# Optimization experiments

Hardware: AMD Instinct MI355X
Metric: run time of the kernel (lower is better)

The kernel has to match this reference:

```python
import jax, jax.numpy as jnp
import numpy as np

TOP_K = 8


def setup_inputs() -> dict:
    key = jax.random.key(0)
    k1, k2 = jax.random.split(key)
    hidden_states = jax.random.normal(k1, (16384, 2048), dtype=jnp.float32)
    weight = jax.random.normal(k2, (64, 2048), dtype=jnp.float32) * 0.02
    return {"hidden_states": hidden_states, "weight": weight}


def reference(hidden_states, weight):
    # router_logits = F.linear(hidden_states, weight): [T, E]
    router_logits = jnp.einsum('th,eh->te', hidden_states, weight)
    # softmax in float32 as in the original
    router_probs = jax.nn.softmax(router_logits.astype(jnp.float32), axis=-1)
    router_top_values, router_indices = jax.lax.top_k(router_probs, TOP_K)
    # norm_topk_prob=True: renormalize selected probs to sum to 1
    router_top_values = router_top_values / jnp.sum(router_top_values, axis=-1, keepdims=True)
    return (router_logits,
            router_top_values.astype(hidden_states.dtype),
            router_indices)
```

## Files before the change

kernel.cpp:

```cpp
#include <hip/hip_runtime.h>
#include <math.h>

#define T_TOKENS 16384
#define HID      2048
#define NE       64
#define TOPK     8
#define TM       32
#define BK       128
#define NCH      (HID / BK)
#define RSTR     272
#define A_SPL    (TM * RSTR)
#define ABUF     (3 * A_SPL)
#define LDS_BYTES (2 * ABUF)

#define WS_SHORT8 49152

typedef float    f32x4  __attribute__((ext_vector_type(4)));
typedef short    short8 __attribute__((ext_vector_type(8)));
typedef unsigned uint4v __attribute__((ext_vector_type(4)));

#define MFMA16(A, B, C) __builtin_amdgcn_mfma_f32_16x16x32_bf16((A), (B), (C), 0, 0, 0)

static __device__ __forceinline__ unsigned short f2bf(float x) {
    unsigned u = __builtin_bit_cast(unsigned, x);
    return (unsigned short)((u + 0x7FFFu + ((u >> 16) & 1u)) >> 16);
}

static __device__ __forceinline__ void split8(const float4 v0, const float4 v1,
                                              uint4v& p0, uint4v& p1, uint4v& p2)
{
    const float x[8] = {v0.x, v0.y, v0.z, v0.w, v1.x, v1.y, v1.z, v1.w};
    #pragma unroll
    for (int j = 0; j < 4; ++j) {
        const float xe = x[2 * j], xo = x[2 * j + 1];
        const unsigned ue  = __builtin_bit_cast(unsigned, xe);
        const unsigned m0e = (ue + 0x8000u) & 0xFFFF0000u;
        const float    r1e = xe - __builtin_bit_cast(float, m0e);
        const unsigned u1e = __builtin_bit_cast(unsigned, r1e);
        const unsigned m1e = (u1e + 0x8000u) & 0xFFFF0000u;
        const float    r2e = r1e - __builtin_bit_cast(float, m1e);
        const unsigned u2e = __builtin_bit_cast(unsigned, r2e);
        const unsigned uo  = __builtin_bit_cast(unsigned, xo);
        const unsigned m0o = (uo + 0x8000u) & 0xFFFF0000u;
        const float    r1o = xo - __builtin_bit_cast(float, m0o);
        const unsigned u1o = __builtin_bit_cast(unsigned, r1o);
        const unsigned m1o = (u1o + 0x8000u) & 0xFFFF0000u;
        const float    r2o = r1o - __builtin_bit_cast(float, m1o);
        const unsigned u2o = __builtin_bit_cast(unsigned, r2o);
        p0[j] = m0o | (m0e >> 16);
        p1[j] = m1o | (m1e >> 16);
        p2[j] = (u2o & 0xFFFF0000u) | (u2e >> 16);
    }
}

__global__ __launch_bounds__(256) void split_weight_kernel(
    const float* __restrict__ weight, uint4v* __restrict__ ws)
{
    const int n = blockIdx.x;
    const int o = threadIdx.x;
    const float4 w0 = *(const float4*)&weight[(size_t)n * HID + o * 8];
    const float4 w1 = *(const float4*)&weight[(size_t)n * HID + o * 8 + 4];
    uint4v p0, p1, p2;
    split8(w0, w1, p0, p1, p2);
    const int t    = o >> 2;
    const int lane = (o & 3) * 16 + (n & 15);
    const int e    = n >> 4;
    const int base = t * 256 + e * 64 + lane;
    ws[base]         = p0;
    ws[base + 16384] = p1;
    ws[base + 32768] = p2;
}

__global__ __launch_bounds__(256, 2) void router_kernel(
    const float* __restrict__ hidden,
    const short8* __restrict__ bfrag,
    float* __restrict__ out_logits,
    float* __restrict__ out_vals,
    float* __restrict__ out_idxf)
{
    __shared__ __align__(16) char smem[LDS_BYTES];
    double (*lg)[NE + 1] = reinterpret_cast<double(*)[NE + 1]>(smem);

    const int tid  = threadIdx.x;
    const int tok0 = blockIdx.x * TM;
    const int lane = tid & 63;
    const int wave = tid >> 6;

    const int fr = lane & 15;
    const int fk = lane >> 4;

    int rowmap[4], colmap[4];
    {
        const unsigned short mb = f2bf((float)fr);
        const unsigned short ob = f2bf(0.03125f);
        short8 vm, vo;
        #pragma unroll
        for (int j = 0; j < 8; ++j) { vm[j] = (short)mb; vo[j] = (short)ob; }
        const f32x4 z = {0.f, 0.f, 0.f, 0.f};
        const f32x4 pr = MFMA16(vm, vo, z);
        const f32x4 pc = MFMA16(vo, vm, z);
        #pragma unroll
        for (int i = 0; i < 4; ++i) {
            rowmap[i] = (int)(pr[i] + 0.5f);
            colmap[i] = (int)(pc[i] + 0.5f);
        }
    }

    const int ar   = tid >> 3;
    const int ac16 = (tid & 7) * 16;
    const float* aG = hidden + (size_t)(tok0 + ar) * HID + ac16;
    const int aWOff = ar * RSTR + ac16 * 2;

    const short8* bP = bfrag + wave * 64 + lane;

    const int aOff0 = fr * RSTR + fk * 16;
    const int aOff1 = (16 + fr) * RSTR + fk * 16;

    const f32x4 z4 = {0.f, 0.f, 0.f, 0.f};
    f32x4 acch[2] = {z4, z4};
    f32x4 accl[2] = {z4, z4};
    double accd[2][4] = {{0, 0, 0, 0}, {0, 0, 0, 0}};

    float4 pa[4];
    short8 Bcur0, Bcur1, Bcur2;

    {
        #pragma unroll
        for (int q = 0; q < 4; ++q) pa[q] = *(const float4*)(aG + 4 * q);
        uint4v p0, p1, p2;
        char* aW = smem + aWOff;
        split8(pa[0], pa[1], p0, p1, p2);
        *(uint4v*)(aW            ) = p0;
        *(uint4v*)(aW +   A_SPL  ) = p1;
        *(uint4v*)(aW + 2*A_SPL  ) = p2;
        split8(pa[2], pa[3], p0, p1, p2);
        *(uint4v*)(aW             + 16) = p0;
        *(uint4v*)(aW +   A_SPL   + 16) = p1;
        *(uint4v*)(aW + 2*A_SPL   + 16) = p2;
    }
    Bcur0 = bP[0];
    Bcur1 = bP[16384];
    Bcur2 = bP[32768];
    __syncthreads();

    for (int c = 0; c < NCH; ++c) {
        const char* bufc = smem + (c & 1) * ABUF;

        short8 A00 = *(const short8*)(bufc + aOff0);
        short8 A01 = *(const short8*)(bufc + A_SPL + aOff0);
        short8 A02 = *(const short8*)(bufc + 2 * A_SPL + aOff0);
        short8 A10 = *(const short8*)(bufc + aOff1);
        short8 A11 = *(const short8*)(bufc + A_SPL + aOff1);
        short8 A12 = *(const short8*)(bufc + 2 * A_SPL + aOff1);

        if (c + 1 < NCH) {
            const int off = (c + 1) * BK;
            #pragma unroll
            for (int q = 0; q < 4; ++q) pa[q] = *(const float4*)(aG + off + 4 * q);
        }

        #pragma unroll
        for (int st = 0; st < 4; ++st) {
            short8 An00, An01, An02, An10, An11, An12;
            short8 Bn0, Bn1, Bn2;
            if (st < 3) {
                const int ao = (st + 1) * 64;
                An00 = *(const short8*)(bufc + aOff0 + ao);
                An01 = *(const short8*)(bufc + A_SPL + aOff0 + ao);
                An02 = *(const short8*)(bufc + 2 * A_SPL + aOff0 + ao);
                An10 = *(const short8*)(bufc + aOff1 + ao);
                An11 = *(const short8*)(bufc + A_SPL + aOff1 + ao);
                An12 = *(const short8*)(bufc + 2 * A_SPL + aOff1 + ao);
                const int t = c * 4 + st + 1;
                Bn0 = bP[t * 256];
                Bn1 = bP[t * 256 + 16384];
                Bn2 = bP[t * 256 + 32768];
            } else if (c + 1 < NCH) {
                const int t = (c + 1) * 4;
                Bn0 = bP[t * 256];
                Bn1 = bP[t * 256 + 16384];
                Bn2 = bP[t * 256 + 32768];
            }

            acch[0] = MFMA16(A00, Bcur0, acch[0]);
            accl[0] = MFMA16(A00, Bcur1, accl[0]);
            accl[0] = MFMA16(A01, Bcur0, accl[0]);
            accl[0] = MFMA16(A01, Bcur1, accl[0]);
            accl[0] = MFMA16(A00, Bcur2, accl[0]);
            accl[0] = MFMA16(A02, Bcur0, accl[0]);
            acch[1] = MFMA16(A10, Bcur0, acch[1]);
            accl[1] = MFMA16(A10, Bcur1, accl[1]);
            accl[1] = MFMA16(A11, Bcur0, accl[1]);
            accl[1] = MFMA16(A11, Bcur1, accl[1]);
            accl[1] = MFMA16(A10, Bcur2, accl[1]);
            accl[1] = MFMA16(A12, Bcur0, accl[1]);

            if (st < 3) {
                A00 = An00; A01 = An01; A02 = An02;
                A10 = An10; A11 = An11; A12 = An12;
                Bcur0 = Bn0; Bcur1 = Bn1; Bcur2 = Bn2;
            } else if (c + 1 < NCH) {
                Bcur0 = Bn0; Bcur1 = Bn1; Bcur2 = Bn2;
            }
        }

        #pragma unroll
        for (int f = 0; f < 2; ++f) {
            #pragma unroll
            for (int i = 0; i < 4; ++i) accd[f][i] += (double)acch[f][i];
            acch[f] = z4;
        }

        if (c + 1 < NCH) {
            uint4v p0, p1, p2;
            char* aW = smem + ((c & 1) ^ 1) * ABUF + aWOff;
            split8(pa[0], pa[1], p0, p1, p2);
            *(uint4v*)(aW            ) = p0;
            *(uint4v*)(aW +   A_SPL  ) = p1;
            *(uint4v*)(aW + 2*A_SPL  ) = p2;
            split8(pa[2], pa[3], p0, p1, p2);
            *(uint4v*)(aW             + 16) = p0;
            *(uint4v*)(aW +   A_SPL   + 16) = p1;
            *(uint4v*)(aW + 2*A_SPL   + 16) = p2;
        }
        __syncthreads();
    }

    #pragma unroll
    for (int f = 0; f < 2; ++f) {
        #pragma unroll
        for (int i = 0; i < 4; ++i) {
            const int trow = f * 16 + rowmap[i];
            const int tok  = tok0 + trow;
            const int e0   = wave * 16 + colmap[i];
            const double l0 = accd[f][i] + (double)accl[f][i];
            out_logits[(size_t)tok * NE + e0] = (float)l0;
            lg[trow][e0] = l0;
        }
    }
    __syncthreads();

    for (int tt = wave; tt < TM; tt += 4) {
        double cur = lg[tt][lane];
        double first = 0.0;
        float  s = 0.f, myv = 0.f;
        int myi = 0;
        #pragma unroll
        for (int i = 0; i < TOPK; ++i) {
            double mv = cur;
            #pragma unroll
            for (int off = 32; off; off >>= 1) {
                const double ov = __shfl_xor(mv, off);
                mv = ov > mv ? ov : mv;
            }
            const unsigned long long m = __ballot(cur == mv);
            const int mi = __ffsll(m) - 1;
            if (i == 0) first = mv;
            const float e = expf((float)(mv - first));
            s += e;
            if (lane == i)  { myv = e; myi = mi; }
            if (lane == mi) cur = -INFINITY;
        }
        if (lane < TOPK) {
            const int tok = tok0 + tt;
            out_vals[(size_t)tok * TOPK + lane] = myv / s;
            out_idxf[(size_t)tok * TOPK + lane] = (float)myi;
        }
    }
}

extern "C" void kernel_launch(void* const* d_in, const int* in_sizes, int n_in,
                              void* d_out, int out_size, void* d_ws, size_t ws_size,
                              hipStream_t stream) {
    const float* hidden = (const float*)d_in[0];
    const float* weight = (const float*)d_in[1];

    float* out        = (float*)d_out;
    float* out_logits = out;
    float* out_vals   = out + (size_t)T_TOKENS * NE;
    float* out_idxf   = out + (size_t)T_TOKENS * NE + (size_t)T_TOKENS * TOPK;

    uint4v* ws = (uint4v*)d_ws;

    hipLaunchKernelGGL(split_weight_kernel, dim3(NE), dim3(256), 0, stream,
                       weight, ws);
    hipLaunchKernelGGL(router_kernel, dim3(T_TOKENS / TM), dim3(256), 0, stream,
                       hidden, (const short8*)ws, out_logits, out_vals, out_idxf);
}
```

Baseline: 221.4 us.

## Interleave A staging layout, split low accumulators, halve top-k wave work

Changes how each thread loads hidden rows: threads now read float4s at a 32-float stride and write 8-byte split chunks at 64-byte spacing, instead of 16 contiguous floats. The intent is better global coalescing and a different LDS bank pattern. The low-order MFMA accumulators are split into two alternating chains to shorten dependent MFMA chains. The top-k epilogue processes two tokens per wave, using 32 lanes each with two candidates per lane, which cuts the shuffle rounds. The layout changes must stay consistent with the fragment read offsets, otherwise results are wrong.

```diff
diff --git a/kernel.cpp b/kernel.cpp
--- a/kernel.cpp
+++ b/kernel.cpp
@@ -18,6 +18,7 @@
 typedef float    f32x4  __attribute__((ext_vector_type(4)));
 typedef short    short8 __attribute__((ext_vector_type(8)));
 typedef unsigned uint4v __attribute__((ext_vector_type(4)));
+typedef unsigned uint2v __attribute__((ext_vector_type(2)));
 
 #define MFMA16(A, B, C) __builtin_amdgcn_mfma_f32_16x16x32_bf16((A), (B), (C), 0, 0, 0)
 
@@ -26,12 +27,12 @@
     return (unsigned short)((u + 0x7FFFu + ((u >> 16) & 1u)) >> 16);
 }
 
-static __device__ __forceinline__ void split8(const float4 v0, const float4 v1,
-                                              uint4v& p0, uint4v& p1, uint4v& p2)
+static __device__ __forceinline__ void split4(const float4 v,
+                                              uint2v& p0, uint2v& p1, uint2v& p2)
 {
-    const float x[8] = {v0.x, v0.y, v0.z, v0.w, v1.x, v1.y, v1.z, v1.w};
+    const float x[4] = {v.x, v.y, v.z, v.w};
     #pragma unroll
-    for (int j = 0; j < 4; ++j) {
+    for (int j = 0; j < 2; ++j) {
         const float xe = x[2 * j], xo = x[2 * j + 1];
         const unsigned ue  = __builtin_bit_cast(unsigned, xe);
         const unsigned m0e = (ue + 0x8000u) & 0xFFFF0000u;
@@ -60,15 +61,16 @@
     const int o = threadIdx.x;
     const float4 w0 = *(const float4*)&weight[(size_t)n * HID + o * 8];
     const float4 w1 = *(const float4*)&weight[(size_t)n * HID + o * 8 + 4];
-    uint4v p0, p1, p2;
-    split8(w0, w1, p0, p1, p2);
+    uint2v a0, a1, a2, b0, b1, b2;
+    split4(w0, a0, a1, a2);
+    split4(w1, b0, b1, b2);
     const int t    = o >> 2;
     const int lane = (o & 3) * 16 + (n & 15);
     const int e    = n >> 4;
     const int base = t * 256 + e * 64 + lane;
-    ws[base]         = p0;
-    ws[base + 16384] = p1;
-    ws[base + 32768] = p2;
+    ws[base]         = uint4v{a0[0], a0[1], b0[0], b0[1]};
+    ws[base + 16384] = uint4v{a1[0], a1[1], b1[0], b1[1]};
+    ws[base + 32768] = uint4v{a2[0], a2[1], b2[0], b2[1]};
 }
 
 __global__ __launch_bounds__(256, 2) void router_kernel(
@@ -106,10 +108,10 @@
         }
     }
 
-    const int ar   = tid >> 3;
-    const int ac16 = (tid & 7) * 16;
-    const float* aG = hidden + (size_t)(tok0 + ar) * HID + ac16;
-    const int aWOff = ar * RSTR + ac16 * 2;
+    const int ar = tid >> 3;
+    const int ag = tid & 7;
+    const float* aG = hidden + (size_t)(tok0 + ar) * HID + 4 * ag;
+    const int aWOff = ar * RSTR + 8 * ag;
 
     const short8* bP = bfrag + wave * 64 + lane;
 
@@ -117,27 +119,28 @@
     const int aOff1 = (16 + fr) * RSTR + fk * 16;
 
     const f32x4 z4 = {0.f, 0.f, 0.f, 0.f};
-    f32x4 acch[2] = {z4, z4};
-    f32x4 accl[2] = {z4, z4};
+    f32x4 acch[2]    = {z4, z4};
+    f32x4 accl[2][2] = {{z4, z4}, {z4, z4}};
     double accd[2][4] = {{0, 0, 0, 0}, {0, 0, 0, 0}};
 
     float4 pa[4];
     short8 Bcur0, Bcur1, Bcur2;
 
-    {
-        #pragma unroll
-        for (int q = 0; q < 4; ++q) pa[q] = *(const float4*)(aG + 4 * q);
-        uint4v p0, p1, p2;
-        char* aW = smem + aWOff;
-        split8(pa[0], pa[1], p0, p1, p2);
-        *(uint4v*)(aW            ) = p0;
-        *(uint4v*)(aW +   A_SPL  ) = p1;
-        *(uint4v*)(aW + 2*A_SPL  ) = p2;
-        split8(pa[2], pa[3], p0, p1, p2);
-        *(uint4v*)(aW             + 16) = p0;
-        *(uint4v*)(aW +   A_SPL   + 16) = p1;
-        *(uint4v*)(aW + 2*A_SPL   + 16) = p2;
-    }
+#define STAGE_A(dstbase) do {                                                     \
+    uint2v q0, q1, q2;                                                            \
+    char* aW_ = (dstbase) + aWOff;                                                \
+    _Pragma("unroll")                                                             \
+    for (int q_ = 0; q_ < 4; ++q_) {                                              \
+        split4(pa[q_], q0, q1, q2);                                               \
+        *(uint2v*)(aW_             + 64 * q_) = q0;                               \
+        *(uint2v*)(aW_ +   A_SPL   + 64 * q_) = q1;                               \
+        *(uint2v*)(aW_ + 2*A_SPL   + 64 * q_) = q2;                               \
+    }                                                                             \
+} while (0)
+
+    #pragma unroll
+    for (int q = 0; q < 4; ++q) pa[q] = *(const float4*)(aG + 32 * q);
+    STAGE_A(smem);
     Bcur0 = bP[0];
     Bcur1 = bP[16384];
     Bcur2 = bP[32768];
@@ -156,7 +159,7 @@
         if (c + 1 < NCH) {
             const int off = (c + 1) * BK;
             #pragma unroll
-            for (int q = 0; q < 4; ++q) pa[q] = *(const float4*)(aG + off + 4 * q);
+            for (int q = 0; q < 4; ++q) pa[q] = *(const float4*)(aG + off + 32 * q);
         }
 
         #pragma unroll
@@ -182,18 +185,19 @@
                 Bn2 = bP[t * 256 + 32768];
             }
 
-            acch[0] = MFMA16(A00, Bcur0, acch[0]);
-            accl[0] = MFMA16(A00, Bcur1, accl[0]);
-            accl[0] = MFMA16(A01, Bcur0, accl[0]);
-            accl[0] = MFMA16(A01, Bcur1, accl[0]);
-            accl[0] = MFMA16(A00, Bcur2, accl[0]);
-            accl[0] = MFMA16(A02, Bcur0, accl[0]);
-            acch[1] = MFMA16(A10, Bcur0, acch[1]);
-            accl[1] = MFMA16(A10, Bcur1, accl[1]);
-            accl[1] = MFMA16(A11, Bcur0, accl[1]);
-            accl[1] = MFMA16(A11, Bcur1, accl[1]);
-            accl[1] = MFMA16(A10, Bcur2, accl[1]);
-            accl[1] = MFMA16(A12, Bcur0, accl[1]);
+            const int e0 = st & 1, e1 = e0 ^ 1;
+            acch[0]     = MFMA16(A00, Bcur0, acch[0]);
+            accl[0][e0] = MFMA16(A00, Bcur1, accl[0][e0]);
+            accl[0][e1] = MFMA16(A01, Bcur0, accl[0][e1]);
+            accl[0][e0] = MFMA16(A01, Bcur1, accl[0][e0]);
+            accl[0][e1] = MFMA16(A00, Bcur2, accl[0][e1]);
+            accl[0][e0] = MFMA16(A02, Bcur0, accl[0][e0]);
+            acch[1]     = MFMA16(A10, Bcur0, acch[1]);
+            accl[1][e0] = MFMA16(A10, Bcur1, accl[1][e0]);
+            accl[1][e1] = MFMA16(A11, Bcur0, accl[1][e1]);
+            accl[1][e0] = MFMA16(A11, Bcur1, accl[1][e0]);
+            accl[1][e1] = MFMA16(A10, Bcur2, accl[1][e1]);
+            accl[1][e0] = MFMA16(A12, Bcur0, accl[1][e0]);
 
             if (st < 3) {
                 A00 = An00; A01 = An01; A02 = An02;
@@ -212,16 +216,7 @@
         }
 
         if (c + 1 < NCH) {
-            uint4v p0, p1, p2;
-            char* aW = smem + ((c & 1) ^ 1) * ABUF + aWOff;
-            split8(pa[0], pa[1], p0, p1, p2);
-            *(uint4v*)(aW            ) = p0;
-            *(uint4v*)(aW +   A_SPL  ) = p1;
-            *(uint4v*)(aW + 2*A_SPL  ) = p2;
-            split8(pa[2], pa[3], p0, p1, p2);
-            *(uint4v*)(aW             + 16) = p0;
-            *(uint4v*)(aW +   A_SPL   + 16) = p1;
-            *(uint4v*)(aW + 2*A_SPL   + 16) = p2;
+            STAGE_A(smem + ((c & 1) ^ 1) * ABUF);
         }
         __syncthreads();
     }
@@ -233,38 +228,49 @@
             const int trow = f * 16 + rowmap[i];
             const int tok  = tok0 + trow;
             const int e0   = wave * 16 + colmap[i];
-            const double l0 = accd[f][i] + (double)accl[f][i];
+            const double l0 = accd[f][i] + (double)accl[f][0][i]
+                                         + (double)accl[f][1][i];
             out_logits[(size_t)tok * NE + e0] = (float)l0;
             lg[trow][e0] = l0;
         }
     }
     __syncthreads();
 
-    for (int tt = wave; tt < TM; tt += 4) {
-        double cur = lg[tt][lane];
-        double first = 0.0;
-        float  s = 0.f, myv = 0.f;
-        int myi = 0;
-        #pragma unroll
-        for (int i = 0; i < TOPK; ++i) {
-            double mv = cur;
+    {
+        const int elo  = lane & 31;
+        const int half = lane >> 5;
+        for (int tp = wave; tp < TM / 2; tp += 4) {
+            const int tok_r = tp * 2 + half;
+            double cur0 = lg[tok_r][elo];
+            double cur1 = lg[tok_r][elo + 32];
+            double first = 0.0;
+            float  s = 0.f, myv = 0.f;
+            int myi = 0;
             #pragma unroll
-            for (int off = 32; off; off >>= 1) {
-                const double ov = __shfl_xor(mv, off);
-                mv = ov > mv ? ov : mv;
-            }
-            const unsigned long long m = __ballot(cur == mv);
-            const int mi = __ffsll(m) - 1;
-            if (i == 0) first = mv;
-            const float e = expf((float)(mv - first));
-            s += e;
-            if (lane == i)  { myv = e; myi = mi; }
-            if (lane == mi) cur = -INFINITY;
-        }
-        if (lane < TOPK) {
-            const int tok = tok0 + tt;
-            out_vals[(size_t)tok * TOPK + lane] = myv / s;
-            out_idxf[(size_t)tok * TOPK + lane] = (float)myi;
+            for (int i = 0; i < TOPK; ++i) {
+                double mv = cur1 > cur0 ? cur1 : cur0;
+                #pragma unroll
+                for (int off = 16; off; off >>= 1) {
+                    const double ov = __shfl_xor(mv, off);
+                    mv = ov > mv ? ov : mv;
+                }
+                const unsigned long long b0 = __ballot(cur0 == mv);
+                const unsigned long long b1 = __ballot(cur1 == mv);
+                const unsigned m0h = (unsigned)(half ? (b0 >> 32) : b0);
+                const unsigned m1h = (unsigned)(half ? (b1 >> 32) : b1);
+                const int mi = m0h ? (__ffs(m0h) - 1) : (32 + __ffs(m1h) - 1);
+                if (i == 0) first = mv;
+                const float e = expf((float)(mv - first));
+                s += e;
+                if (elo == i)      { myv = e; myi = mi; }
+                if (mi == elo)          cur0 = -INFINITY;
+                else if (mi == elo + 32) cur1 = -INFINITY;
+            }
+            if (elo < TOPK) {
+                const int tok = tok0 + tok_r;
+                out_vals[(size_t)tok * TOPK + elo] = myv / s;
+                out_idxf[(size_t)tok * TOPK + elo] = (float)myi;
+            }
         }
     }
 }
```

Result: slower. 243.5 us (+10.0%).

## Split top-k into separate kernel and deepen B-fragment prefetch to two steps

Applied to the files above, without the earlier changes.

When the workspace is large enough, the GEMM kernel writes double-precision logits to a global workspace and a separate top-k kernel does the softmax/top-k selection, removing the per-block LDS barrier and serial top-k tail from the GEMM kernel. The B-fragment loads are also prefetched two steps ahead instead of one to hide global-load latency. This adds an extra 8 MB double write and read plus a kernel launch, and uses more registers for the deeper prefetch, which could hurt occupancy.

```diff
diff --git a/kernel.cpp b/kernel.cpp
--- a/kernel.cpp
+++ b/kernel.cpp
@@ -13,7 +13,9 @@
 #define ABUF     (3 * A_SPL)
 #define LDS_BYTES (2 * ABUF)
 
-#define WS_SHORT8 49152
+#define WS_B_BYTES  786432
+#define WS_LG_OFF   786432
+#define WS_NEEDED   (WS_LG_OFF + (size_t)T_TOKENS * NE * 8)
 
 typedef float    f32x4  __attribute__((ext_vector_type(4)));
 typedef short    short8 __attribute__((ext_vector_type(8)));
@@ -71,9 +73,11 @@
     ws[base + 32768] = p2;
 }
 
+template<bool FUSED>
 __global__ __launch_bounds__(256, 2) void router_kernel(
     const float* __restrict__ hidden,
     const short8* __restrict__ bfrag,
+    double* __restrict__ lgws,
     float* __restrict__ out_logits,
     float* __restrict__ out_vals,
     float* __restrict__ out_idxf)
@@ -123,6 +127,7 @@
 
     float4 pa[4];
     short8 Bcur0, Bcur1, Bcur2;
+    short8 Bnx0, Bnx1, Bnx2;
 
     {
         #pragma unroll
@@ -141,6 +146,9 @@
     Bcur0 = bP[0];
     Bcur1 = bP[16384];
     Bcur2 = bP[32768];
+    Bnx0  = bP[256];
+    Bnx1  = bP[256 + 16384];
+    Bnx2  = bP[256 + 32768];
     __syncthreads();
 
     for (int c = 0; c < NCH; ++c) {
@@ -162,7 +170,6 @@
         #pragma unroll
         for (int st = 0; st < 4; ++st) {
             short8 An00, An01, An02, An10, An11, An12;
-            short8 Bn0, Bn1, Bn2;
             if (st < 3) {
                 const int ao = (st + 1) * 64;
                 An00 = *(const short8*)(bufc + aOff0 + ao);
@@ -171,15 +178,13 @@
                 An10 = *(const short8*)(bufc + aOff1 + ao);
                 An11 = *(const short8*)(bufc + A_SPL + aOff1 + ao);
                 An12 = *(const short8*)(bufc + 2 * A_SPL + aOff1 + ao);
-                const int t = c * 4 + st + 1;
-                Bn0 = bP[t * 256];
-                Bn1 = bP[t * 256 + 16384];
-                Bn2 = bP[t * 256 + 32768];
-            } else if (c + 1 < NCH) {
-                const int t = (c + 1) * 4;
-                Bn0 = bP[t * 256];
-                Bn1 = bP[t * 256 + 16384];
-                Bn2 = bP[t * 256 + 32768];
+            }
+            short8 B20 = Bnx0, B21 = Bnx1, B22 = Bnx2;
+            if (c < NCH - 1 || st < 2) {
+                const int t2 = (c * 4 + st + 2) * 256;
+                B20 = bP[t2];
+                B21 = bP[t2 + 16384];
+                B22 = bP[t2 + 32768];
             }
 
             acch[0] = MFMA16(A00, Bcur0, acch[0]);
@@ -198,10 +203,9 @@
             if (st < 3) {
                 A00 = An00; A01 = An01; A02 = An02;
                 A10 = An10; A11 = An11; A12 = An12;
-                Bcur0 = Bn0; Bcur1 = Bn1; Bcur2 = Bn2;
-            } else if (c + 1 < NCH) {
-                Bcur0 = Bn0; Bcur1 = Bn1; Bcur2 = Bn2;
-            }
+            }
+            Bcur0 = Bnx0; Bcur1 = Bnx1; Bcur2 = Bnx2;
+            Bnx0  = B20;  Bnx1  = B21;  Bnx2  = B22;
         }
 
         #pragma unroll
@@ -226,22 +230,73 @@
         __syncthreads();
     }
 
-    #pragma unroll
-    for (int f = 0; f < 2; ++f) {
-        #pragma unroll
-        for (int i = 0; i < 4; ++i) {
-            const int trow = f * 16 + rowmap[i];
-            const int tok  = tok0 + trow;
-            const int e0   = wave * 16 + colmap[i];
-            const double l0 = accd[f][i] + (double)accl[f][i];
-            out_logits[(size_t)tok * NE + e0] = (float)l0;
-            lg[trow][e0] = l0;
-        }
-    }
-    __syncthreads();
-
-    for (int tt = wave; tt < TM; tt += 4) {
-        double cur = lg[tt][lane];
+    if constexpr (!FUSED) {
+        #pragma unroll
+        for (int f = 0; f < 2; ++f) {
+            #pragma unroll
+            for (int i = 0; i < 4; ++i) {
+                const int trow = f * 16 + rowmap[i];
+                const int tok  = tok0 + trow;
+                const int e0   = wave * 16 + colmap[i];
+                const double l0 = accd[f][i] + (double)accl[f][i];
+                out_logits[(size_t)tok * NE + e0] = (float)l0;
+                lgws[(size_t)tok * NE + e0]       = l0;
+            }
+        }
+    } else {
+        #pragma unroll
+        for (int f = 0; f < 2; ++f) {
+            #pragma unroll
+            for (int i = 0; i < 4; ++i) {
+                const int trow = f * 16 + rowmap[i];
+                const int tok  = tok0 + trow;
+                const int e0   = wave * 16 + colmap[i];
+                const double l0 = accd[f][i] + (double)accl[f][i];
+                out_logits[(size_t)tok * NE + e0] = (float)l0;
+                lg[trow][e0] = l0;
+            }
+        }
+        __syncthreads();
+
+        for (int tt = wave; tt < TM; tt += 4) {
+            double cur = lg[tt][lane];
+            double first = 0.0;
+            float  s = 0.f, myv = 0.f;
+            int myi = 0;
+            #pragma unroll
+            for (int i = 0; i < TOPK; ++i) {
+                double mv = cur;
+                #pragma unroll
+                for (int off = 32; off; off >>= 1) {
+                    const double ov = __shfl_xor(mv, off);
+                    mv = ov > mv ? ov : mv;
+                }
+                const unsigned long long m = __ballot(cur == mv);
+                const int mi = __ffsll(m) - 1;
+                if (i == 0) first = mv;
+                const float e = expf((float)(mv - first));
+                s += e;
+                if (lane == i)  { myv = e; myi = mi; }
+                if (lane == mi) cur = -INFINITY;
+            }
+            if (lane < TOPK) {
+                const int tok = tok0 + tt;
+                out_vals[(size_t)tok * TOPK + lane] = myv / s;
+                out_idxf[(size_t)tok * TOPK + lane] = (float)myi;
+            }
+        }
+    }
+}
+
+__global__ __launch_bounds__(256) void topk_kernel(
+    const double* __restrict__ lgws,
+    float* __restrict__ out_vals,
+    float* __restrict__ out_idxf)
+{
+    const int lane = threadIdx.x & 63;
+    const int gw   = (blockIdx.x * 256 + threadIdx.x) >> 6;
+    for (int tok = gw; tok < T_TOKENS; tok += 4096) {
+        double cur = lgws[(size_t)tok * NE + lane];
         double first = 0.0;
         float  s = 0.f, myv = 0.f;
         int myi = 0;
@@ -262,7 +317,6 @@
             if (lane == mi) cur = -INFINITY;
         }
         if (lane < TOPK) {
-            const int tok = tok0 + tt;
             out_vals[(size_t)tok * TOPK + lane] = myv / s;
             out_idxf[(size_t)tok * TOPK + lane] = (float)myi;
         }
@@ -280,10 +334,21 @@
     float* out_vals   = out + (size_t)T_TOKENS * NE;
     float* out_idxf   = out + (size_t)T_TOKENS * NE + (size_t)T_TOKENS * TOPK;
 
-    uint4v* ws = (uint4v*)d_ws;
+    uint4v* ws   = (uint4v*)d_ws;
+    double* lgws = (double*)((char*)d_ws + WS_LG_OFF);
 
     hipLaunchKernelGGL(split_weight_kernel, dim3(NE), dim3(256), 0, stream,
                        weight, ws);
-    hipLaunchKernelGGL(router_kernel, dim3(T_TOKENS / TM), dim3(256), 0, stream,
-                       hidden, (const short8*)ws, out_logits, out_vals, out_idxf);
-}
+
+    if (ws_size >= WS_NEEDED) {
+        hipLaunchKernelGGL((router_kernel<false>), dim3(T_TOKENS / TM), dim3(256),
+                           0, stream, hidden, (const short8*)ws, lgws,
+                           out_logits, out_vals, out_idxf);
+        hipLaunchKernelGGL(topk_kernel, dim3(1024), dim3(256), 0, stream,
+                           lgws, out_vals, out_idxf);
+    } else {
+        hipLaunchKernelGGL((router_kernel<true>), dim3(T_TOKENS / TM), dim3(256),
+                           0, stream, hidden, (const short8*)ws, (double*)nullptr,
+                           out_logits, out_vals, out_idxf);
+    }
+}
```

New measurement: 219.2 us. Within noise of the previous version (-1.0%).
